# Kernel tuning notes

Measured on AMD Instinct MI355X. Metric: run time of the kernel, lower is better.

## Reference

```python
import jax, jax.numpy as jnp
import numpy as np

EMB = 1024
HEADS = 16
HEAD_DIM = EMB // HEADS
B, T = 2, 2048
LN_EPS = 1e-5  # torch nn.LayerNorm default


def _layernorm(x, g, b):
    # LayerNorm over last dim (head_dim), elementwise affine
    mu = jnp.mean(x, axis=-1, keepdims=True)
    var = jnp.mean(jnp.square(x - mu), axis=-1, keepdims=True)
    return (x - mu) * jax.lax.rsqrt(var + LN_EPS) * g + b


def setup_inputs() -> dict:
    key = jax.random.key(0)
    ks = jax.random.split(key, 6)
    sc = 1.0 / np.sqrt(EMB)  # keep linear outputs O(1)
    return {
        "x": jax.random.normal(ks[0], (B, T, EMB), dtype=jnp.float32),
        "Wk": jax.random.normal(ks[1], (EMB, EMB), dtype=jnp.float32) * sc,
        "Wq": jax.random.normal(ks[2], (EMB, EMB), dtype=jnp.float32) * sc,
        "Wv": jax.random.normal(ks[3], (EMB, EMB), dtype=jnp.float32) * sc,
        "Wu": jax.random.normal(ks[4], (EMB, EMB), dtype=jnp.float32) * sc,
        "bu": jnp.zeros((EMB,), dtype=jnp.float32),
        "kln_g": jnp.ones((HEAD_DIM,), dtype=jnp.float32),
        "kln_b": jnp.zeros((HEAD_DIM,), dtype=jnp.float32),
        "qln_g": jnp.ones((HEAD_DIM,), dtype=jnp.float32),
        "qln_b": jnp.zeros((HEAD_DIM,), dtype=jnp.float32),
    }


def reference(x, Wk, Wq, Wv, Wu, bu, kln_g, kln_b, qln_g, qln_b):
    b, t, e = x.shape
    h, s = HEADS, HEAD_DIM
    # torch Linear (no bias): y = x @ W.T
    keys = (x @ Wk.T).reshape(b, t, h, s)
    queries = (x @ Wq.T).reshape(b, t, h, s)
    values = (x @ Wv.T).reshape(b, t, h, s)
    # per-head LayerNorm (kqnorm=True)
    keys = _layernorm(keys, kln_g, kln_b)
    queries = _layernorm(queries, qln_g, qln_b)
    # NOTE: module scales by emb**(-1/4) on each side (net 1/sqrt(emb), not head dim)
    inv4 = e ** (-0.25)
    queries = queries * inv4
    keys = keys * inv4
    # scores: [b, h, t, t]
    dot = jnp.einsum('bqhs,bkhs->bhqk', queries, keys)
    # causal mask: positions k > q set to -inf (mask_diagonal=False -> diag kept)
    causal = jnp.tril(jnp.ones((t, t), dtype=bool))
    dot = jnp.where(causal, dot, -jnp.inf)
    attn = jax.nn.softmax(dot, axis=-1)
    out = jnp.einsum('bhqk,bkhs->bqhs', attn, values).reshape(b, t, h * s)
    return out @ Wu.T + bu
```

## Files before the change

### kernel.cpp

```cpp
#include <hip/hip_runtime.h>
#include <math.h>

#define EMB 1024
#define NHEADS 16
#define HDIM 64
#define BATCH 2
#define SEQ 2048
#define MROWS (BATCH*SEQ)
#define LN_EPS 1e-5f
#define GK 1024
#define GN 1024

typedef __attribute__((ext_vector_type(8))) short bf16x8;
typedef __attribute__((ext_vector_type(4))) short s16x4;
typedef __attribute__((ext_vector_type(4))) float f32x4;
typedef __attribute__((ext_vector_type(16))) float f32x16;
typedef __attribute__((ext_vector_type(4))) int int4v;

__device__ __forceinline__ short f2bf(float f) {
    union { float f; unsigned u; } v; v.f = f;
    unsigned r = v.u + 0x7FFFu + ((v.u >> 16) & 1u);
    return (short)(r >> 16);
}
__device__ __forceinline__ float bf2f(short s) {
    union { unsigned u; float f; } v; v.u = ((unsigned)(unsigned short)s) << 16;
    return v.f;
}
__device__ __forceinline__ unsigned cvtpk(float a, float b) {
    unsigned r;
    asm("v_cvt_pk_bf16_f32 %0, %1, %2" : "=v"(r) : "v"(a), "v"(b));
    return r;
}
__device__ __forceinline__ float fexp2(float x) {
    return __builtin_amdgcn_exp2f(x);
}

__device__ __forceinline__ void gload16(const short* g, short* l) {
    __builtin_amdgcn_global_load_lds(
        (const __attribute__((address_space(1))) unsigned*)g,
        (__attribute__((address_space(3))) unsigned*)l, 16, 0, 0);
}

#define MFMA32(a, b, c) __builtin_amdgcn_mfma_f32_32x32x16_bf16(a, b, c, 0, 0, 0)

#define SRC_G(r, c)  ((((c) - ((r) >> 1)) & 3) * 8)
#define RD_G(r, l4)  ((((l4) + ((r) >> 1)) & 3) * 8)

__global__ __launch_bounds__(256)
void cvt_all(const float* __restrict__ X, short* __restrict__ XH,
             const float* __restrict__ W0, const float* __restrict__ W1,
             const float* __restrict__ W2, const float* __restrict__ W3,
             short* __restrict__ WH)
{
    const int zy = blockIdx.y;
    if (zy == 0) {
        const size_t i = (size_t)blockIdx.x * 1024 + threadIdx.x * 4;
        const float4 v = *(const float4*)&X[i];
        s16x4 h;
        h[0] = f2bf(v.x); h[1] = f2bf(v.y);
        h[2] = f2bf(v.z); h[3] = f2bf(v.w);
        *(s16x4*)&XH[i] = h;
    } else {
        const int z = zy - 1;
        if (blockIdx.x >= 1024) return;
        const float* W = (z == 0) ? W0 : (z == 1) ? W1 : (z == 2) ? W2 : W3;
        const size_t i = (size_t)blockIdx.x * 1024 + threadIdx.x * 4;
        const float4 v = *(const float4*)&W[i];
        s16x4 h;
        h[0] = f2bf(v.x); h[1] = f2bf(v.y);
        h[2] = f2bf(v.z); h[3] = f2bf(v.w);
        *(s16x4*)&WH[((size_t)z << 20) + i] = h;
    }
}

__global__ __launch_bounds__(256, 3)
void gemm_kqv(const short* __restrict__ Xh, const short* __restrict__ W4h,
              const float* __restrict__ kg, const float* __restrict__ kb,
              const float* __restrict__ qg, const float* __restrict__ qb,
              float scaleK, float scaleQ,
              short* __restrict__ KhP, short* __restrict__ QhP,
              short* __restrict__ VTh)
{
    __shared__ short AhS[3][128][32], BhS[3][128][32];

    const int t   = threadIdx.x;
    const int ln  = t & 63, wv = t >> 6;
    const int l15 = ln & 15, l4 = ln >> 4;
    const int m0  = blockIdx.y * 128;
    const int n0  = blockIdx.x * 128;
    const int z   = blockIdx.z;
    const int wr  = (wv >> 1) * 64, wc = (wv & 1) * 64;

    const short* Bh = W4h + ((size_t)z << 20);

    const short* gplane = (wv < 2) ? Xh : Bh;
    const int    grow0  = (wv < 2) ? m0 : n0;
    short* lbase = (wv < 2) ? &AhS[0][0][0] : &BhS[0][0][0];
    const int s0 = (wv & 1) ? 4 : 0;

    f32x4 acc[4][4];
    #pragma unroll
    for (int i = 0; i < 4; ++i)
        #pragma unroll
        for (int j = 0; j < 4; ++j) acc[i][j] = (f32x4){0.f, 0.f, 0.f, 0.f};

    #pragma unroll
    for (int s = 0; s < 4; ++s) {
        const int chunk = (s0 + s) * 64 + ln;
        const int r = chunk >> 2, c = chunk & 3;
        gload16(gplane + (size_t)(grow0 + r) * GK + SRC_G(r, c),
                lbase + (s0 + s) * 512);
    }
    #pragma unroll
    for (int s = 0; s < 4; ++s) {
        const int chunk = (s0 + s) * 64 + ln;
        const int r = chunk >> 2, c = chunk & 3;
        gload16(gplane + (size_t)(grow0 + r) * GK + 32 + SRC_G(r, c),
                lbase + 4096 + (s0 + s) * 512);
    }
    asm volatile("s_waitcnt vmcnt(4)" ::: "memory");
    __builtin_amdgcn_s_barrier();

    int cur = 0;
    for (int i = 0; i < 32; ++i) {
        const int cur2 = (cur == 0) ? 2 : cur - 1;
        if (i + 2 < 32) {
            short* lp = lbase + cur2 * 4096;
            const int kof = (i + 2) * 32;
            #pragma unroll
            for (int s = 0; s < 4; ++s) {
                const int chunk = (s0 + s) * 64 + ln;
                const int r = chunk >> 2, c = chunk & 3;
                gload16(gplane + (size_t)(grow0 + r) * GK + kof + SRC_G(r, c),
                        lp + (s0 + s) * 512);
            }
        }

        bf16x8 ah[4], bh[4];
        #pragma unroll
        for (int f = 0; f < 4; ++f) {
            const int ra = wr + f * 16 + l15;
            const int rb = wc + f * 16 + l15;
            ah[f] = *(const bf16x8*)&AhS[cur][ra][RD_G(ra, l4)];
            bh[f] = *(const bf16x8*)&BhS[cur][rb][RD_G(rb, l4)];
        }
        #pragma unroll
        for (int i2 = 0; i2 < 4; ++i2)
            #pragma unroll
            for (int j = 0; j < 4; ++j)
                acc[i2][j] = __builtin_amdgcn_mfma_f32_16x16x32_bf16(ah[i2], bh[j], acc[i2][j], 0, 0, 0);

        if (i + 2 < 32) {
            asm volatile("s_waitcnt vmcnt(4)" ::: "memory");
        } else if (i + 1 < 32) {
            asm volatile("s_waitcnt vmcnt(0)" ::: "memory");
        }
        __builtin_amdgcn_s_barrier();
        cur = (cur == 2) ? 0 : cur + 1;
    }

    if (z < 2) {
        const float* gamma = (z == 0) ? kg : qg;
        const float* beta  = (z == 0) ? kb : qb;
        short* OutH = (z == 0) ? KhP : QhP;
        const float scl = (z == 0) ? scaleK : scaleQ;
        const int n_head = (n0 + wc) >> 6;
        float g4[4], b4[4];
        #pragma unroll
        for (int f = 0; f < 4; ++f) {
            g4[f] = gamma[f * 16 + l15];
            b4[f] = beta [f * 16 + l15];
        }
        #pragma unroll
        for (int i = 0; i < 4; ++i)
            #pragma unroll
            for (int j = 0; j < 4; ++j) {
                const float v0 = acc[i][0][j], v1 = acc[i][1][j];
                const float v2 = acc[i][2][j], v3 = acc[i][3][j];
                float s1 = v0 + v1 + v2 + v3;
                float s2 = v0*v0 + v1*v1 + v2*v2 + v3*v3;
                s1 += __shfl_xor(s1, 1); s2 += __shfl_xor(s2, 1);
                s1 += __shfl_xor(s1, 2); s2 += __shfl_xor(s2, 2);
                s1 += __shfl_xor(s1, 4); s2 += __shfl_xor(s2, 4);
                s1 += __shfl_xor(s1, 8); s2 += __shfl_xor(s2, 8);
                const float mu  = s1 * (1.f / 64.f);
                const float var = s2 * (1.f / 64.f) - mu * mu;
                const float rs  = rsqrtf(var + LN_EPS);
                const int m = m0 + wr + i * 16 + l4 * 4 + j;
                const size_t orow =
                    ((size_t)((m >> 11) * NHEADS + n_head) * SEQ + (m & (SEQ - 1))) * HDIM;
                #pragma unroll
                for (int f = 0; f < 4; ++f) {
                    const float y = ((acc[i][f][j] - mu) * rs * g4[f] + b4[f]) * scl;
                    OutH[orow + f * 16 + l15] = f2bf(y);
                }
            }
    } else {
        #pragma unroll
        for (int i = 0; i < 4; ++i)
            #pragma unroll
            for (int f = 0; f < 4; ++f) {
                s16x4 h4;
                #pragma unroll
                for (int j = 0; j < 4; ++j) h4[j] = f2bf(acc[i][f][j]);
                const int n  = n0 + wc + f * 16 + l15;
                const int hh = n >> 6, dd = n & 63;
                const int mb = m0 + wr + i * 16 + l4 * 4;
                const size_t oa =
                    (((size_t)((mb >> 11) * NHEADS + hh)) * HDIM + dd) * SEQ + (mb & (SEQ - 1));
                *(s16x4*)&VTh[oa] = h4;
            }
    }
}

__global__ __launch_bounds__(256, 2)
void gemm_out(const short* __restrict__ Ah, const short* __restrict__ Bh,
              const float* __restrict__ bias, float* __restrict__ OutF)
{
    __shared__ short AhS[2][64][32], BhS[2][128][32];

    const int t   = threadIdx.x;
    const int ln  = t & 63, wv = t >> 6;
    const int l15 = ln & 15, l4 = ln >> 4;
    const int m0  = blockIdx.y * 64;
    const int n0  = blockIdx.x * 128;
    const int wr  = (wv >> 1) * 32, wc = (wv & 1) * 64;

    const short* gplane = (wv == 0) ? Ah : Bh;
    const int    grow0  = (wv == 0) ? m0 : n0;
    const int    s0     = (wv == 2) ? 4 : 0;
    const int    nseg   = (wv < 3) ? 4 : 0;
    const int    bstep  = (wv == 0) ? 2048 : 4096;
    short* lbase = (wv == 0) ? &AhS[0][0][0] : &BhS[0][0][0];

    f32x4 acc[2][4];
    #pragma unroll
    for (int i = 0; i < 2; ++i)
        #pragma unroll
        for (int j = 0; j < 4; ++j) acc[i][j] = (f32x4){0.f, 0.f, 0.f, 0.f};

    for (int s = 0; s < nseg; ++s) {
        const int chunk = (s0 + s) * 64 + ln;
        const int r = chunk >> 2, c = chunk & 3;
        gload16(gplane + (size_t)(grow0 + r) * GK + SRC_G(r, c),
                lbase + (s0 + s) * 512);
    }
    __syncthreads();

    int cur = 0;
    for (int k0 = 0; k0 < GK; k0 += 32) {
        if (k0 + 32 < GK) {
            short* lp = lbase + (cur ^ 1) * bstep;
            for (int s = 0; s < nseg; ++s) {
                const int chunk = (s0 + s) * 64 + ln;
                const int r = chunk >> 2, c = chunk & 3;
                gload16(gplane + (size_t)(grow0 + r) * GK + k0 + 32 + SRC_G(r, c),
                        lp + (s0 + s) * 512);
            }
        }

        bf16x8 ah[2], bh[4];
        #pragma unroll
        for (int f = 0; f < 2; ++f) {
            const int ra = wr + f * 16 + l15;
            ah[f] = *(const bf16x8*)&AhS[cur][ra][RD_G(ra, l4)];
        }
        #pragma unroll
        for (int f = 0; f < 4; ++f) {
            const int rb = wc + f * 16 + l15;
            bh[f] = *(const bf16x8*)&BhS[cur][rb][RD_G(rb, l4)];
        }
        #pragma unroll
        for (int i = 0; i < 2; ++i)
            #pragma unroll
            for (int j = 0; j < 4; ++j)
                acc[i][j] = __builtin_amdgcn_mfma_f32_16x16x32_bf16(ah[i], bh[j], acc[i][j], 0, 0, 0);

        __syncthreads();
        cur ^= 1;
    }

    float b4[4];
    #pragma unroll
    for (int f = 0; f < 4; ++f) b4[f] = bias[n0 + wc + f * 16 + l15];
    #pragma unroll
    for (int i = 0; i < 2; ++i)
        #pragma unroll
        for (int j = 0; j < 4; ++j) {
            const int m = m0 + wr + i * 16 + l4 * 4 + j;
            const size_t row = (size_t)m * GN + n0 + wc;
            #pragma unroll
            for (int f = 0; f < 4; ++f)
                OutF[row + f * 16 + l15] = acc[i][f][j] + b4[f];
        }
}

__global__ __launch_bounds__(512, 4)
void attn_mfma(const short* __restrict__ Qh, const short* __restrict__ Kh,
               const short* __restrict__ Vh, short* __restrict__ Oh)
{
    __shared__ short KhS[2][64][64];
    __shared__ short VhS[2][64][64];

    const int t    = threadIdx.x;
    const int lane = t & 63, wv = t >> 6;
    const int l31  = lane & 31, hb = lane >> 5;
    const int stripe = wv & 3, kh2 = wv >> 2;

    const int lin = (int)blockIdx.y * 16 + (int)blockIdx.x;
    const int xcd = lin & 7;
    const int m   = lin >> 3;
    const int bh  = xcd * 4 + (m >> 4);
    const int qtr = m & 15;
    const int qt  = ((m >> 5) & 1) ? qtr : 15 - qtr;

    const int bb   = bh >> 4, hh = bh & 15;
    const int q0   = qt * 128;
    const int wq0  = stripe * 32;

    const size_t kpan = (size_t)bh * SEQ * HDIM;
    const size_t vpan = (size_t)bh * HDIM * SEQ;

    const int u    = t & 255, u8 = t >> 8;
    const int sr0  = u >> 3, sr1 = 32 + (u >> 3);
    const int scg  = u & 7;
    const int soff = scg * 8;
    const int lc0  = (scg ^ (sr0 & 7)) * 8;

    bf16x8 qfh[4];
    {
        const size_t qrow = kpan + (size_t)(q0 + wq0 + l31) * HDIM;
        #pragma unroll
        for (int ds = 0; ds < 4; ++ds)
            qfh[ds] = *(const bf16x8*)&Qh[qrow + ds * 16 + hb * 8];
    }

    f32x16 oacc0 = (f32x16)(0.0f), oacc1 = (f32x16)(0.0f);
    float m_run = -1e30f, l_run = 0.f;

    const int NR = qt + 1;

    int4v pK0, pK1, pV0, pV1;
    {
        const int kb0 = u8 * 64;
        pK0 = *(const int4v*)&Kh[kpan + (size_t)(kb0 + sr0) * HDIM + soff];
        pK1 = *(const int4v*)&Kh[kpan + (size_t)(kb0 + sr1) * HDIM + soff];
        pV0 = *(const int4v*)&Vh[vpan + (size_t)sr0 * SEQ + kb0 + soff];
        pV1 = *(const int4v*)&Vh[vpan + (size_t)sr1 * SEQ + kb0 + soff];
    }

    for (int rr = 0; rr < NR; ++rr) {
        const int k0 = rr * 128;

        __syncthreads();

        *(int4v*)&KhS[u8][sr0][lc0] = pK0;
        *(int4v*)&KhS[u8][sr1][lc0] = pK1;
        *(int4v*)&VhS[u8][sr0][lc0] = pV0;
        *(int4v*)&VhS[u8][sr1][lc0] = pV1;

        if (rr + 1 < NR) {
            const int kb0 = k0 + 128 + u8 * 64;
            pK0 = *(const int4v*)&Kh[kpan + (size_t)(kb0 + sr0) * HDIM + soff];
            pK1 = *(const int4v*)&Kh[kpan + (size_t)(kb0 + sr1) * HDIM + soff];
            pV0 = *(const int4v*)&Vh[vpan + (size_t)sr0 * SEQ + kb0 + soff];
            pV1 = *(const int4v*)&Vh[vpan + (size_t)sr1 * SEQ + kb0 + soff];
        }
        __syncthreads();

        #pragma unroll
        for (int half = 0; half < 2; ++half) {
            const int kw0 = k0 + half * 64 + kh2 * 32;
            if (kw0 > q0 + wq0 + 31) continue;

            f32x16 s = (f32x16)(0.0f);
            #pragma unroll
            for (int ds = 0; ds < 4; ++ds) {
                const int g = ((ds * 2 + hb) ^ (l31 & 7)) * 8;
                const bf16x8 kf = *(const bf16x8*)&KhS[half][kh2 * 32 + l31][g];
                s = MFMA32(kf, qfh[ds], s);
            }

            if (kw0 + 31 > q0 + wq0) {
                const int qg = q0 + wq0 + l31;
                #pragma unroll
                for (int reg = 0; reg < 16; ++reg) {
                    const int kk = kw0 + (reg & 3) + 8 * (reg >> 2) + 4 * hb;
                    if (kk > qg) s[reg] = -1e30f;
                }
            }

            {
                const float a0 = fmaxf(s[0], s[1]),  a1 = fmaxf(s[2], s[3]);
                const float a2 = fmaxf(s[4], s[5]),  a3 = fmaxf(s[6], s[7]);
                const float a4 = fmaxf(s[8], s[9]),  a5 = fmaxf(s[10], s[11]);
                const float a6 = fmaxf(s[12], s[13]), a7 = fmaxf(s[14], s[15]);
                const float b0 = fmaxf(a0, a1), b1 = fmaxf(a2, a3);
                const float b2 = fmaxf(a4, a5), b3 = fmaxf(a6, a7);
                float mx = fmaxf(fmaxf(b0, b1), fmaxf(b2, b3));
                mx = fmaxf(mx, __shfl_xor(mx, 32));
                if (__any(mx > m_run)) {
                    const float mnew = fmaxf(m_run, mx);
                    const float scf  = fexp2(m_run - mnew);
                    m_run = mnew;
                    l_run *= scf;
                    #pragma unroll
                    for (int reg = 0; reg < 16; ++reg) {
                        oacc0[reg] *= scf;
                        oacc1[reg] *= scf;
                    }
                }
                #pragma unroll
                for (int reg = 0; reg < 16; ++reg)
                    s[reg] = fexp2(s[reg] - m_run);
                const float c0 = (s[0] + s[1]) + (s[2] + s[3]);
                const float c1 = (s[4] + s[5]) + (s[6] + s[7]);
                const float c2 = (s[8] + s[9]) + (s[10] + s[11]);
                const float c3 = (s[12] + s[13]) + (s[14] + s[15]);
                float ls = (c0 + c1) + (c2 + c3);
                ls += __shfl_xor(ls, 32);
                l_run += ls;
            }

            #pragma unroll
            for (int ks2 = 0; ks2 < 2; ++ks2) {
                const int ks = kh2 * 2 + ks2;
                const int sb = ks2 * 8;
                const unsigned hA0 = cvtpk(s[sb + 0], s[sb + 1]);
                const unsigned hA1 = cvtpk(s[sb + 2], s[sb + 3]);
                const unsigned hB0 = cvtpk(s[sb + 4], s[sb + 5]);
                const unsigned hB1 = cvtpk(s[sb + 6], s[sb + 7]);
                const unsigned hr0 = (unsigned)__shfl_xor((int)(hb ? hA0 : hB0), 32);
                const unsigned hr1 = (unsigned)__shfl_xor((int)(hb ? hA1 : hB1), 32);
                const int4v wih = (int4v){(int)(hb ? hr0 : hA0), (int)(hb ? hr1 : hA1),
                                          (int)(hb ? hB0 : hr0), (int)(hb ? hB1 : hr1)};
                const bf16x8 pfh = __builtin_bit_cast(bf16x8, wih);

                const int gv = ((ks * 2 + hb) ^ (l31 & 7)) * 8;
                const bf16x8 vh0 = *(const bf16x8*)&VhS[half][l31][gv];
                const bf16x8 vh1 = *(const bf16x8*)&VhS[half][32 + l31][gv];
                oacc0 = MFMA32(vh0, pfh, oacc0);
                oacc1 = MFMA32(vh1, pfh, oacc1);
            }
        }
    }

    __syncthreads();
    unsigned* oscr = (unsigned*)&KhS[0][0][0];
    float*    mls  = (float*)&VhS[0][0][0];
    const int cbase = (stripe * 64 + lane) * 16;
    const int crot  = lane >> 1;

    if (kh2 == 1) {
        #pragma unroll
        for (int i = 0; i < 8; ++i)
            oscr[cbase + ((i + crot) & 15)]       = cvtpk(oacc0[2 * i], oacc0[2 * i + 1]);
        #pragma unroll
        for (int i = 0; i < 8; ++i)
            oscr[cbase + ((8 + i + crot) & 15)]   = cvtpk(oacc1[2 * i], oacc1[2 * i + 1]);
        mls[(stripe * 64 + lane) * 2]     = m_run;
        mls[(stripe * 64 + lane) * 2 + 1] = l_run;
    }
    __syncthreads();

    if (kh2 == 0) {
        const float mB = mls[(stripe * 64 + lane) * 2];
        const float lB = mls[(stripe * 64 + lane) * 2 + 1];
        const float mm = fmaxf(m_run, mB);
        const float fa = fexp2(m_run - mm);
        const float fb = fexp2(mB - mm);
        const float inv = 1.f / (l_run * fa + lB * fb);

        const int q = q0 + wq0 + l31;
        const size_t row = ((size_t)(bb * SEQ + q)) * EMB + hh * HDIM;
        #pragma unroll
        for (int db = 0; db < 2; ++db)
            #pragma unroll
            for (int b = 0; b < 4; ++b) {
                const int pi = db * 8 + 2 * b;
                const unsigned uB0 = oscr[cbase + ((pi + crot) & 15)];
                const unsigned uB1 = oscr[cbase + ((pi + 1 + crot) & 15)];
                const float a0 = (db ? oacc1[4 * b + 0] : oacc0[4 * b + 0]);
                const float a1 = (db ? oacc1[4 * b + 1] : oacc0[4 * b + 1]);
                const float a2 = (db ? oacc1[4 * b + 2] : oacc0[4 * b + 2]);
                const float a3 = (db ? oacc1[4 * b + 3] : oacc0[4 * b + 3]);
                const float v0 = (a0 * fa + bf2f((short)(uB0 & 0xffff))  * fb) * inv;
                const float v1 = (a1 * fa + bf2f((short)(uB0 >> 16))    * fb) * inv;
                const float v2 = (a2 * fa + bf2f((short)(uB1 & 0xffff)) * fb) * inv;
                const float v3 = (a3 * fa + bf2f((short)(uB1 >> 16))    * fb) * inv;
                uint2 w2;
                w2.x = cvtpk(v0, v1);
                w2.y = cvtpk(v2, v3);
                const int d0 = db * 32 + 8 * b + 4 * hb;
                *(uint2*)&Oh[row + d0] = w2;
            }
    }
}

extern "C" void kernel_launch(void* const* d_in, const int* in_sizes, int n_in,
                              void* d_out, int out_size, void* d_ws, size_t ws_size,
                              hipStream_t stream)
{
    const float* x  = (const float*)d_in[0];
    const float* Wk = (const float*)d_in[1];
    const float* Wq = (const float*)d_in[2];
    const float* Wv = (const float*)d_in[3];
    const float* Wu = (const float*)d_in[4];
    const float* bu = (const float*)d_in[5];
    const float* kg = (const float*)d_in[6];
    const float* kb = (const float*)d_in[7];
    const float* qg = (const float*)d_in[8];
    const float* qb = (const float*)d_in[9];
    float* out = (float*)d_out;

    char* w = (char*)d_ws;
    short* XhP = (short*)(w);
    short* KhP = (short*)(w + (8u  << 20));
    short* QhP = (short*)(w + (16u << 20));
    short* W4h = (short*)(w + (24u << 20));
    short* VTh = (short*)d_out;

    const float inv4 = 0.17677669529663687f;
    const float l2e  = 1.4426950408889634f;

    cvt_all<<<dim3(4096, 5), 256, 0, stream>>>(x, XhP, Wk, Wq, Wv, Wu, W4h);

    gemm_kqv<<<dim3(GN / 128, MROWS / 128, 3), 256, 0, stream>>>(
        XhP, W4h, kg, kb, qg, qb, inv4, inv4 * l2e,
        KhP, QhP, VTh);

    attn_mfma<<<dim3(SEQ / 128, BATCH * NHEADS), 512, 0, stream>>>(
        QhP, KhP, VTh, XhP);

    gemm_out<<<dim3(GN / 128, MROWS / 64), 256, 0, stream>>>(
        XhP, W4h + (3u << 20), bu, out);
}
```

Baseline: 109.3 us.

## Shrink QKV GEMM tile to 64x128 with double buffering and more blocks

Halves the M tile of the fused K/Q/V projection GEMM from 128 to 64 rows and doubles the grid. The three-stage async LDS pipeline with fine-grained vmcnt waits becomes a two-stage double buffer guarded by __syncthreads. Wave 3 no longer loads, and each wave holds half the accumulators. The aim is more blocks and higher occupancy (launch bounds 4), at the cost of less data reuse per block, more global traffic, and a shallower prefetch.

```diff
diff --git a/kernel.cpp b/kernel.cpp
--- a/kernel.cpp
+++ b/kernel.cpp
@@ -73,7 +73,7 @@
     }
 }
 
-__global__ __launch_bounds__(256, 3)
+__global__ __launch_bounds__(256, 4)
 void gemm_kqv(const short* __restrict__ Xh, const short* __restrict__ W4h,
               const float* __restrict__ kg, const float* __restrict__ kb,
               const float* __restrict__ qg, const float* __restrict__ qb,
@@ -81,82 +81,70 @@
               short* __restrict__ KhP, short* __restrict__ QhP,
               short* __restrict__ VTh)
 {
-    __shared__ short AhS[3][128][32], BhS[3][128][32];
+    __shared__ short AhS[2][64][32], BhS[2][128][32];
 
     const int t   = threadIdx.x;
     const int ln  = t & 63, wv = t >> 6;
     const int l15 = ln & 15, l4 = ln >> 4;
-    const int m0  = blockIdx.y * 128;
+    const int m0  = blockIdx.y * 64;
     const int n0  = blockIdx.x * 128;
     const int z   = blockIdx.z;
-    const int wr  = (wv >> 1) * 64, wc = (wv & 1) * 64;
+    const int wr  = (wv >> 1) * 32, wc = (wv & 1) * 64;
 
     const short* Bh = W4h + ((size_t)z << 20);
 
-    const short* gplane = (wv < 2) ? Xh : Bh;
-    const int    grow0  = (wv < 2) ? m0 : n0;
-    short* lbase = (wv < 2) ? &AhS[0][0][0] : &BhS[0][0][0];
-    const int s0 = (wv & 1) ? 4 : 0;
-
-    f32x4 acc[4][4];
+    const short* gplane = (wv == 0) ? Xh : Bh;
+    const int    grow0  = (wv == 0) ? m0 : n0;
+    const int    s0     = (wv == 2) ? 4 : 0;
+    const int    nseg   = (wv < 3) ? 4 : 0;
+    const int    bstep  = (wv == 0) ? 2048 : 4096;
+    short* lbase = (wv == 0) ? &AhS[0][0][0] : &BhS[0][0][0];
+
+    f32x4 acc[2][4];
     #pragma unroll
-    for (int i = 0; i < 4; ++i)
+    for (int i = 0; i < 2; ++i)
         #pragma unroll
         for (int j = 0; j < 4; ++j) acc[i][j] = (f32x4){0.f, 0.f, 0.f, 0.f};
 
-    #pragma unroll
-    for (int s = 0; s < 4; ++s) {
+    for (int s = 0; s < nseg; ++s) {
         const int chunk = (s0 + s) * 64 + ln;
         const int r = chunk >> 2, c = chunk & 3;
         gload16(gplane + (size_t)(grow0 + r) * GK + SRC_G(r, c),
                 lbase + (s0 + s) * 512);
     }
-    #pragma unroll
-    for (int s = 0; s < 4; ++s) {
-        const int chunk = (s0 + s) * 64 + ln;
-        const int r = chunk >> 2, c = chunk & 3;
-        gload16(gplane + (size_t)(grow0 + r) * GK + 32 + SRC_G(r, c),
-                lbase + 4096 + (s0 + s) * 512);
-    }
-    asm volatile("s_waitcnt vmcnt(4)" ::: "memory");
-    __builtin_amdgcn_s_barrier();
+    __syncthreads();
 
     int cur = 0;
-    for (int i = 0; i < 32; ++i) {
-        const int cur2 = (cur == 0) ? 2 : cur - 1;
-        if (i + 2 < 32) {
-            short* lp = lbase + cur2 * 4096;
-            const int kof = (i + 2) * 32;
-            #pragma unroll
-            for (int s = 0; s < 4; ++s) {
+    for (int k0 = 0; k0 < GK; k0 += 32) {
+        if (k0 + 32 < GK) {
+            short* lp = lbase + (cur ^ 1) * bstep;
+            for (int s = 0; s < nseg; ++s) {
                 const int chunk = (s0 + s) * 64 + ln;
                 const int r = chunk >> 2, c = chunk & 3;
-                gload16(gplane + (size_t)(grow0 + r) * GK + kof + SRC_G(r, c),
+                gload16(gplane + (size_t)(grow0 + r) * GK + k0 + 32 + SRC_G(r, c),
                         lp + (s0 + s) * 512);
             }
         }
 
-        bf16x8 ah[4], bh[4];
+        bf16x8 ah[2], bh[4];
+        #pragma unroll
+        for (int f = 0; f < 2; ++f) {
+            const int ra = wr + f * 16 + l15;
+            ah[f] = *(const bf16x8*)&AhS[cur][ra][RD_G(ra, l4)];
+        }
         #pragma unroll
         for (int f = 0; f < 4; ++f) {
-            const int ra = wr + f * 16 + l15;
             const int rb = wc + f * 16 + l15;
-            ah[f] = *(const bf16x8*)&AhS[cur][ra][RD_G(ra, l4)];
             bh[f] = *(const bf16x8*)&BhS[cur][rb][RD_G(rb, l4)];
         }
         #pragma unroll
-        for (int i2 = 0; i2 < 4; ++i2)
+        for (int i = 0; i < 2; ++i)
             #pragma unroll
             for (int j = 0; j < 4; ++j)
-                acc[i2][j] = __builtin_amdgcn_mfma_f32_16x16x32_bf16(ah[i2], bh[j], acc[i2][j], 0, 0, 0);
-
-        if (i + 2 < 32) {
-            asm volatile("s_waitcnt vmcnt(4)" ::: "memory");
-        } else if (i + 1 < 32) {
-            asm volatile("s_waitcnt vmcnt(0)" ::: "memory");
-        }
-        __builtin_amdgcn_s_barrier();
-        cur = (cur == 2) ? 0 : cur + 1;
+                acc[i][j] = __builtin_amdgcn_mfma_f32_16x16x32_bf16(ah[i], bh[j], acc[i][j], 0, 0, 0);
+
+        __syncthreads();
+        cur ^= 1;
     }
 
     if (z < 2) {
@@ -172,7 +160,7 @@
             b4[f] = beta [f * 16 + l15];
         }
         #pragma unroll
-        for (int i = 0; i < 4; ++i)
+        for (int i = 0; i < 2; ++i)
             #pragma unroll
             for (int j = 0; j < 4; ++j) {
                 const float v0 = acc[i][0][j], v1 = acc[i][1][j];
@@ -197,7 +185,7 @@
             }
     } else {
         #pragma unroll
-        for (int i = 0; i < 4; ++i)
+        for (int i = 0; i < 2; ++i)
             #pragma unroll
             for (int f = 0; f < 4; ++f) {
                 s16x4 h4;
@@ -525,7 +513,7 @@
 
     cvt_all<<<dim3(4096, 5), 256, 0, stream>>>(x, XhP, Wk, Wq, Wv, Wu, W4h);
 
-    gemm_kqv<<<dim3(GN / 128, MROWS / 128, 3), 256, 0, stream>>>(
+    gemm_kqv<<<dim3(GN / 128, MROWS / 64, 3), 256, 0, stream>>>(
         XhP, W4h, kg, kb, qg, qb, inv4, inv4 * l2e,
         KhP, QhP, VTh);
 
```

Result: slower. 119.4 us (+9.2%).
